# Kernel tuning notes

Hardware: AMD Instinct MI355X
Metric: run time of the kernel (lower is better)

Reference implementation:

```python
import jax, jax.numpy as jnp
import numpy as np

B, CIN, D, H, W = 2, 64, 64, 64, 64
NUM_CLASSES = 5
STRIDE = 2
NMAX = 32
TOPK = 13
TAL_ALPHA, TAL_BETA = 1.0, 6.0
EPS = 1e-9


def setup_inputs() -> dict:
    key = jax.random.key(0)
    ks = jax.random.split(key, 6)
    features = jax.random.normal(ks[0], (B, CIN, D, H, W), jnp.float32)
    cls_w = jax.random.normal(ks[1], (NUM_CLASSES, CIN, 3, 3, 3), jnp.float32) * 0.02
    cls_b = jnp.zeros((NUM_CLASSES,), jnp.float32)
    off_w = jax.random.normal(ks[2], (3, CIN, 3, 3, 3), jnp.float32) * 0.01
    off_b = jnp.zeros((3,), jnp.float32)
    coords = jax.random.uniform(ks[3], (B, NMAX, 3), jnp.float32, 4.0, float(D * STRIDE) - 4.0)
    cls = jax.random.randint(ks[4], (B, NMAX, 1), 0, NUM_CLASSES).astype(jnp.float32)
    sigma = jax.random.uniform(ks[5], (B, NMAX, 1), jnp.float32, 2.0, 8.0)
    pad = (jnp.arange(NMAX) >= 24)[None, :, None]  # last 8 GT slots are padding
    cls = jnp.where(pad, -100.0, cls)
    labels = jnp.concatenate([coords, cls, sigma], axis=-1)  # B N 5 : x,y,z,class,sigma
    return {"features": features, "cls_w": cls_w, "cls_b": cls_b,
            "off_w": off_w, "off_b": off_b, "labels": labels}


def conv3d(x, w, b):
    y = jax.lax.conv_general_dilated(x, w, (1, 1, 1), 'SAME',
                                     dimension_numbers=('NCDHW', 'OIDHW', 'NCDHW'))
    return y + b[None, :, None, None, None]


def make_anchors():
    g = jnp.stack(jnp.meshgrid(jnp.arange(D), jnp.arange(H), jnp.arange(W), indexing='ij'))
    return (g.astype(jnp.float32) + 0.5) * STRIDE  # (3, D, H, W)


def flatten_bchw(x):
    # B C D H W -> B (D H W) C
    Bsz, C = x.shape[0], x.shape[1]
    return x.transpose(0, 2, 3, 4, 1).reshape(Bsz, -1, C)


def tal_assign(pred_logits, pred_centers, true_labels, true_centers, true_sigmas, valid):
    # pred_logits (B,L,C); pred_centers (B,L,3); true_* (B,N,...); valid (B,N) bool
    Bsz, L, C = pred_logits.shape
    N = true_labels.shape[1]
    d2 = jnp.sum((true_centers[:, :, None, :] - pred_centers[:, None, :, :]) ** 2, -1)  # B N L
    ious = jnp.exp(-d2 / (2.0 * true_sigmas[:, :, None] ** 2))  # keypoint IoU, B N L
    probs = jax.nn.sigmoid(pred_logits).transpose(0, 2, 1)  # B C L
    cls_scores = jnp.take_along_axis(probs, true_labels[:, :, None], axis=1)  # B N L
    align = (cls_scores ** TAL_ALPHA) * (ious ** TAL_BETA)  # alignment metric
    topv, topi = jax.lax.top_k(align, TOPK)
    is_topk = jnp.zeros_like(align).at[
        jnp.arange(Bsz)[:, None, None], jnp.arange(N)[None, :, None], topi
    ].set(jnp.where(topv > EPS, 1.0, 0.0))
    mask_pos = is_topk * valid[:, :, None].astype(align.dtype)  # B N L
    pos_sum = mask_pos.sum(axis=1)  # B L
    # resolve anchors matched to multiple GTs: keep GT with max IoU
    is_max_iou = jax.nn.one_hot(jnp.argmax(ious, axis=1), N, axis=1, dtype=align.dtype)
    mask_pos = jnp.where(pos_sum[:, None, :] > 1, is_max_iou, mask_pos)
    pos_sum = mask_pos.sum(axis=1)
    fg = pos_sum > 0  # B L
    assigned_gt = jnp.argmax(mask_pos, axis=1)  # B L
    assigned_labels = jnp.take_along_axis(true_labels, assigned_gt, axis=1)
    assigned_labels = jnp.where(fg, assigned_labels, C)  # bg_index = C
    assigned_centers = jnp.take_along_axis(true_centers, assigned_gt[:, :, None], axis=1)  # B L 3
    assigned_sigmas = jnp.take_along_axis(true_sigmas, assigned_gt, axis=1)  # B L
    align = align * mask_pos
    max_align = align.max(axis=2, keepdims=True)  # B N 1
    max_iou = (ious * mask_pos).max(axis=2, keepdims=True)
    score = (align * max_iou / (max_align + EPS)).max(axis=1)  # B L
    assigned_scores = jax.nn.one_hot(assigned_labels, C + 1)[..., :C] * score[..., None]  # B L C
    return assigned_labels, assigned_centers, assigned_scores, assigned_sigmas


def detection_loss(logits, offsets, anchors, labels):
    pred_logits = flatten_bchw(logits)               # B L C
    pred_centers = flatten_bchw(anchors + offsets)   # B L 3
    anchor_pts = flatten_bchw(anchors)
    C = pred_logits.shape[-1]
    true_centers = labels[..., :3]
    true_labels_f = labels[..., 3]
    true_sigmas = labels[..., 4]
    valid = true_labels_f != -100.0
    true_labels = jnp.where(valid, true_labels_f, 0.0).astype(jnp.int32)
    assigned = tal_assign(jax.lax.stop_gradient(pred_logits),
                          jax.lax.stop_gradient(pred_centers),
                          true_labels, true_centers, true_sigmas, valid)
    assigned_labels, assigned_centers, assigned_scores, assigned_sigmas = jax.lax.stop_gradient(assigned)
    one_hot_label = jax.nn.one_hot(assigned_labels, C + 1)[..., :C]
    # varifocal loss (alpha=0.75, gamma=2)
    p = jax.nn.sigmoid(pred_logits)
    weight = 0.75 * (p ** 2.0) * (1.0 - one_hot_label) + assigned_scores * one_hot_label
    bce = assigned_scores * jax.nn.softplus(-pred_logits) + (1.0 - assigned_scores) * jax.nn.softplus(pred_logits)
    cls_loss = jnp.sum(weight * bce)
    d = jnp.sum((pred_centers - assigned_centers) ** 2, -1)  # B L
    w = assigned_scores.sum(-1)
    iou = jnp.exp(-d / (2.0 * assigned_sigmas ** 2))
    mask_positive = assigned_labels != C
    reg_loss = jnp.sum(jnp.where(mask_positive, (1.0 - iou) * w, 0.0))
    return (cls_loss + reg_loss) / assigned_scores.sum()


def reference(features, cls_w, cls_b, off_w, off_b, labels):
    logits = conv3d(features, cls_w, cls_b)    # B C D H W
    offsets = conv3d(features, off_w, off_b)   # B 3 D H W
    anchors = jnp.broadcast_to(make_anchors()[None], (features.shape[0], 3, D, H, W))
    loss = detection_loss(logits, offsets, anchors, labels)
    return loss
```

## Files before the change

kernel.cpp:

```cpp
#include <hip/hip_runtime.h>
#include <math.h>

#define NB 2
#define CIN 64
#define DD_ 64
#define HH_ 64
#define WW_ 64
#define NCLS 5
#define LL (DD_*HH_*WW_)
#define NMAXG 32
#define TOPKK 13
#define NSLAB 4

typedef __attribute__((ext_vector_type(8)))  short short8b;
typedef __attribute__((ext_vector_type(16))) float floatx16;

__device__ __forceinline__ float softplusf_(float z){
  return fmaxf(z, 0.f) + log1pf(expf(-fabsf(z)));
}
__device__ __forceinline__ float sigmoidf_(float z){
  return 1.f/(1.f + expf(-z));
}
__device__ __forceinline__ unsigned tobf_u_(float f){
  unsigned u = __float_as_uint(f);
  return (u + 0x7fffu + ((u>>16)&1u)) >> 16;
}
__device__ __forceinline__ short tobf_(float f){
  return (short)tobf_u_(f);
}

__global__ __launch_bounds__(256) void wtrans_kernel(
    const float* __restrict__ cls_w, const float* __restrict__ off_w,
    short* __restrict__ wA, float* __restrict__ bgz)
{
  if (blockIdx.x == 0 && threadIdx.x < 2) bgz[threadIdx.x] = 0.f;
  int idx = blockIdx.x*256 + threadIdx.x;
  if (idx >= 216*64) return;
  int slice = idx >> 6; int lane = idx & 63;
  int cc = slice & 3; int r = slice >> 2;
  int kw = r % 3; int r2 = r / 3;
  int kh = r2 % 3; int rr = r2 / 3;
  int m = lane & 31, khalf = lane >> 5;
  int outch = m & 7;
  int kd = rr - (m >> 3);
  short8b out;
  #pragma unroll
  for (int i=0;i<8;++i){
    int c = cc*16 + khalf*8 + i;
    float wv = 0.f;
    if (kd >= 0 && kd <= 2){
      if (outch < NCLS) wv = cls_w[(outch*CIN + c)*27 + kd*9 + kh*3 + kw];
      else              wv = off_w[((outch-NCLS)*CIN + c)*27 + kd*9 + kh*3 + kw];
    }
    out[i] = tobf_(wv);
  }
  *(short8b*)(wA + (size_t)idx*8) = out;
}

__global__ __launch_bounds__(256) void transpose_kernel(
    const float* __restrict__ feat, short* __restrict__ featT)
{
  const int t = threadIdx.x;
  const int w = t & 63;
  const int hh = t >> 6;
  const int d = blockIdx.x;
  const int h = blockIdx.y*4 + hh;
  const int b = blockIdx.z;
  const float* src = feat + (size_t)b*CIN*LL + (size_t)d*4096 + (size_t)h*64 + w;
  const size_t sp = (size_t)d*4096 + (size_t)h*64 + w;
  #pragma unroll
  for (int cc=0; cc<4; ++cc){
    float f[16];
    #pragma unroll
    for (int j=0;j<16;++j) f[j] = src[(size_t)(cc*16+j)*LL];
    uint4 p0, p1;
    p0.x = (tobf_u_(f[1])<<16)|tobf_u_(f[0]);  p0.y = (tobf_u_(f[3])<<16)|tobf_u_(f[2]);
    p0.z = (tobf_u_(f[5])<<16)|tobf_u_(f[4]);  p0.w = (tobf_u_(f[7])<<16)|tobf_u_(f[6]);
    p1.x = (tobf_u_(f[9])<<16)|tobf_u_(f[8]);  p1.y = (tobf_u_(f[11])<<16)|tobf_u_(f[10]);
    p1.z = (tobf_u_(f[13])<<16)|tobf_u_(f[12]);p1.w = (tobf_u_(f[15])<<16)|tobf_u_(f[14]);
    short* dst = featT + ((size_t)(b*4+cc)*LL + sp)*16;
    *(uint4*)(dst)     = p0;
    *(uint4*)(dst + 8) = p1;
  }
}

__global__ __launch_bounds__(256, 2) void conv_mfma_kernel(
    const short* __restrict__ featT,
    const short* __restrict__ wA,
    const float* __restrict__ cls_b, const float* __restrict__ off_b,
    float* __restrict__ logits_ws,
    float* __restrict__ centers_ws,
    float* __restrict__ bg_sum,
    unsigned* __restrict__ moff_u)
{
  __shared__ short xs[36*68*16];
  __shared__ float bsum[4];

  const int tid = threadIdx.x;
  const int lane = tid & 63, hl = tid >> 6;
  const int col = lane & 31, khalf = lane >> 5;
  const int h0 = blockIdx.x*4, d0 = blockIdx.y*4, b = blockIdx.z;

  for (int idx = tid; idx < 36*32; idx += 256){
    int row = idx >> 5; int rr2 = idx & 31;
    int wp = (rr2 < 16) ? 0 : 65;
    xs[(row*68 + wp)*16 + (rr2 & 15)] = 0;
  }

  floatx16 accA = (floatx16)(0.f);
  floatx16 accB = (floatx16)(0.f);

  const short8b* wAv = (const short8b*)wA;
  const bool edge = (d0==0) || (d0==DD_-4) || (h0==0) || (h0==HH_-4);

  #pragma unroll 1
  for (int cc=0; cc<4; ++cc){
    if (cc) __syncthreads();
    const short* plane = featT + (size_t)(b*4+cc)*LL*16;
    if (!edge){
      #pragma unroll 3
      for (int it=0; it<18; ++it){
        int idx = it*256 + tid;
        int half = idx & 1;
        int wp1  = ((idx>>1) & 63) + 1;
        int row  = idx >> 7;
        int row_d = row/6, row_h = row - row_d*6;
        const short* sp = plane + ((size_t)(d0-1+row_d)*4096 + (size_t)(h0-1+row_h)*64 + (wp1-1))*16 + half*8;
        uint4 pk = *(const uint4*)sp;
        *(uint4*)(xs + (row*68 + wp1)*16 + ((half ^ ((wp1>>2)&1))<<3)) = pk;
      }
    } else {
      #pragma unroll 3
      for (int it=0; it<18; ++it){
        int idx = it*256 + tid;
        int half = idx & 1;
        int wp1  = ((idx>>1) & 63) + 1;
        int row  = idx >> 7;
        int row_d = row/6, row_h = row - row_d*6;
        int d_ = d0 - 1 + row_d;
        int h_ = h0 - 1 + row_h;
        bool inb = ((unsigned)d_ < 64u) && ((unsigned)h_ < 64u);
        const short* sp = plane + ((size_t)(inb?d_:0)*4096 + (size_t)(inb?h_:0)*64 + (wp1-1))*16 + half*8;
        uint4 pk = make_uint4(0,0,0,0);
        if (inb) pk = *(const uint4*)sp;
        *(uint4*)(xs + (row*68 + wp1)*16 + ((half ^ ((wp1>>2)&1))<<3)) = pk;
      }
    }
    __syncthreads();
    #pragma unroll 1
    for (int rr=0; rr<6; ++rr){
      if ((unsigned)(d0 - 1 + rr) >= 64u) continue;
      short8b areg[9];
      #pragma unroll
      for (int q=0;q<9;++q)
        areg[q] = wAv[(size_t)((rr*9 + q)*4 + cc)*64 + lane];
      #pragma unroll
      for (int kh=0;kh<3;++kh){
        if ((unsigned)(h0 + hl - 1 + kh) >= 64u) continue;
        int row = rr*6 + hl + kh;
        #pragma unroll
        for (int kw=0;kw<3;++kw){
          short8b a = areg[kh*3+kw];
          {
            int wp = col + kw;
            int sidx = (row*68 + wp)*16 + ((khalf ^ ((wp>>2)&1))<<3);
            short8b bfr = *(const short8b*)(xs + sidx);
            accA = __builtin_amdgcn_mfma_f32_32x32x16_bf16(a, bfr, accA, 0,0,0);
          }
          {
            int wp = 32 + col + kw;
            int sidx = (row*68 + wp)*16 + ((khalf ^ ((wp>>2)&1))<<3);
            short8b bfr = *(const short8b*)(xs + sidx);
            accB = __builtin_amdgcn_mfma_f32_32x32x16_bf16(a, bfr, accB, 0,0,0);
          }
        }
      }
    }
  }

  float bg = 0.f, om = 0.f;
  const int h = h0 + hl;
  #pragma unroll
  for (int wh=0; wh<2; ++wh){
    const int w = wh*32 + col;
    #pragma unroll
    for (int dq=0; dq<4; ++dq){
      int d = d0 + dq;
      size_t l = (size_t)d*4096 + (size_t)h*64 + w;
      float v0 = wh ? accB[dq*4+0] : accA[dq*4+0];
      float v1 = wh ? accB[dq*4+1] : accA[dq*4+1];
      float v2 = wh ? accB[dq*4+2] : accA[dq*4+2];
      float v3 = wh ? accB[dq*4+3] : accA[dq*4+3];
      if (khalf == 0){
        float z0 = v0 + cls_b[0]; logits_ws[(size_t)(b*NCLS+0)*LL + l] = z0;
        float z1 = v1 + cls_b[1]; logits_ws[(size_t)(b*NCLS+1)*LL + l] = z1;
        float z2 = v2 + cls_b[2]; logits_ws[(size_t)(b*NCLS+2)*LL + l] = z2;
        float z3 = v3 + cls_b[3]; logits_ws[(size_t)(b*NCLS+3)*LL + l] = z3;
        float p;
        p = sigmoidf_(z0); bg += 0.75f*p*p*softplusf_(z0);
        p = sigmoidf_(z1); bg += 0.75f*p*p*softplusf_(z1);
        p = sigmoidf_(z2); bg += 0.75f*p*p*softplusf_(z2);
        p = sigmoidf_(z3); bg += 0.75f*p*p*softplusf_(z3);
      } else {
        float z4 = v0 + cls_b[4]; logits_ws[(size_t)(b*NCLS+4)*LL + l] = z4;
        float p = sigmoidf_(z4); bg += 0.75f*p*p*softplusf_(z4);
        float o0 = v1 + off_b[0];
        float o1 = v2 + off_b[1];
        float o2 = v3 + off_b[2];
        om = fmaxf(om, fmaxf(fabsf(o0), fmaxf(fabsf(o1), fabsf(o2))));
        float4 ctr;
        ctr.x = ((float)d+0.5f)*2.f + o0;
        ctr.y = ((float)h+0.5f)*2.f + o1;
        ctr.z = ((float)w+0.5f)*2.f + o2;
        ctr.w = 0.f;
        *(float4*)(centers_ws + ((size_t)b*LL + l)*4) = ctr;
      }
    }
  }
  #pragma unroll
  for (int off=32;off;off>>=1){
    bg += __shfl_down(bg, off);
    om = fmaxf(om, __shfl_xor(om, off));
  }
  if (lane == 0){
    bsum[hl] = bg;
    atomicMax(moff_u, __float_as_uint(om));
  }
  __syncthreads();
  if (tid == 0)
    atomicAdd(bg_sum, bsum[0]+bsum[1]+bsum[2]+bsum[3]);
}

__global__ __launch_bounds__(256) void topk_box_kernel(
    const float* __restrict__ logits_ws, const float* __restrict__ centers_ws,
    const float* __restrict__ labels,
    const unsigned* __restrict__ moff_u,
    float* __restrict__ pv, int* __restrict__ pi)
{
  const int bn = blockIdx.x;
  const int slab = blockIdx.y;
  const int b = bn >> 5, n = bn & 31;
  const int tid = threadIdx.x;

  const float* lb = labels + (b*NMAXG + n)*5;
  const float tx = lb[0], ty = lb[1], tz = lb[2];
  const float cf = lb[3];
  const float sg = lb[4];
  const int lab = (cf == -100.f) ? 0 : (int)cf;
  const float m6 = -3.f/(sg*sg);
  const float moff = __uint_as_float(*moff_u);
  const float R = 2.6336f*sg + moff + 0.05f;

  int i0d = (int)ceilf((tx - R - 1.f)*0.5f); if (i0d < 0) i0d = 0;
  int i1d = (int)floorf((tx + R - 1.f)*0.5f); if (i1d > 63) i1d = 63;
  int i0h = (int)ceilf((ty - R - 1.f)*0.5f); if (i0h < 0) i0h = 0;
  int i1h = (int)floorf((ty + R - 1.f)*0.5f); if (i1h > 63) i1h = 63;
  int i0w = (int)ceilf((tz - R - 1.f)*0.5f); if (i0w < 0) i0w = 0;
  int i1w = (int)floorf((tz + R - 1.f)*0.5f); if (i1w > 63) i1w = 63;
  int nd = i1d-i0d+1, nh = i1h-i0h+1, nw = i1w-i0w+1;
  int total = (nd>0 && nh>0 && nw>0) ? nd*nh*nw : 0;
  int lo = (total*slab)/NSLAB, hi = (total*(slab+1))/NSLAB;

  const float* lg = logits_ws + (size_t)(b*NCLS + lab)*LL;
  const float* cb = centers_ws + (size_t)b*LL*4;

  float v[13]; int ix[13];
  #pragma unroll
  for (int j=0;j<13;++j){ v[j]=-1.f; ix[j]=0x7fffffff; }

  for (int idx = lo + tid; idx < hi; idx += 256){
    int r = idx;
    int wi = r % nw; r /= nw;
    int hi2 = r % nh; int di = r / nh;
    int l = (i0d+di)*4096 + (i0h+hi2)*64 + (i0w+wi);
    float4 c4 = *(const float4*)(cb + (size_t)l*4);
    float dx = c4.x-tx, dy = c4.y-ty, dz = c4.z-tz;
    float e = m6*(dx*dx + dy*dy + dz*dz);
    if (e < -20.8f) continue;
    float a = sigmoidf_(lg[l]) * expf(e);
    if (a > v[12]){
      float cv = a; int ci = l;
      #pragma unroll
      for (int j=0;j<13;++j){
        bool take = (cv > v[j]) || (cv == v[j] && ci < ix[j]);
        float nv = take ? cv : v[j];  float ov = take ? v[j] : cv;
        int   ni = take ? ci : ix[j]; int   oi = take ? ix[j] : ci;
        v[j]=nv; ix[j]=ni; cv=ov; ci=oi;
      }
    }
  }

  const int lane = tid & 63, wvi = tid >> 6;
  float mv = -2.f; int mi = 0x7fffffff;
  #pragma unroll 1
  for (int k=0;k<13;++k){
    float bv = v[0]; int bi = ix[0]; int bl = lane;
    #pragma unroll
    for (int off=32; off; off>>=1){
      float ov2 = __shfl_xor(bv, off);
      int oi = __shfl_xor(bi, off);
      int ol = __shfl_xor(bl, off);
      if (ov2 > bv || (ov2 == bv && oi < bi)){ bv=ov2; bi=oi; bl=ol; }
    }
    if (lane == k){ mv = bv; mi = bi; }
    if (lane == bl){
      #pragma unroll
      for (int j=0;j<12;++j){ v[j]=v[j+1]; ix[j]=ix[j+1]; }
      v[12] = -2.f; ix[12] = 0x7fffffff;
    }
  }
  __shared__ float sv2[4*13]; __shared__ int si2[4*13];
  if (lane < 13){ sv2[wvi*13+lane] = mv; si2[wvi*13+lane] = mi; }
  __syncthreads();
  if (wvi == 0){
    float v2 = -2.f; int i2 = 0x7fffffff;
    if (lane < 52){ v2 = sv2[lane]; i2 = si2[lane]; }
    #pragma unroll 1
    for (int k=0;k<13;++k){
      float bv = v2; int bi = i2; int bl = lane;
      #pragma unroll
      for (int off=32; off; off>>=1){
        float ov2 = __shfl_xor(bv, off);
        int oi = __shfl_xor(bi, off);
        int ol = __shfl_xor(bl, off);
        if (ov2 > bv || (ov2 == bv && oi < bi)){ bv=ov2; bi=oi; bl=ol; }
      }
      if (lane == 0){
        pv[(bn*NSLAB+slab)*TOPKK + k] = bv;
        pi[(bn*NSLAB+slab)*TOPKK + k] = bi;
      }
      if (lane == bl) v2 = -2.f;
    }
  }
}

__global__ __launch_bounds__(64) void topk_merge_kernel(
    const float* __restrict__ pv, const int* __restrict__ pi,
    float* __restrict__ tv, int* __restrict__ ti)
{
  const int bn = blockIdx.x;
  const int t = threadIdx.x;
  const int NC = NSLAB*TOPKK;
  float v = -2.f; int ix = 0x7fffffff;
  if (t < NC){ v = pv[bn*NC + t]; ix = pi[bn*NC + t]; }
  #pragma unroll 1
  for (int k=0;k<13;++k){
    float bv = v; int bi = ix; int bl = t;
    #pragma unroll
    for (int off=32; off; off>>=1){
      float ov = __shfl_xor(bv, off);
      int oi = __shfl_xor(bi, off);
      int ol = __shfl_xor(bl, off);
      if (ov > bv || (ov == bv && oi < bi)){ bv=ov; bi=oi; bl=ol; }
    }
    if (t==0){ tv[bn*TOPKK+k]=bv; ti[bn*TOPKK+k]=bi; }
    if (t==bl) v = -2.f;
  }
}

__global__ __launch_bounds__(1024) void finalize_kernel(
    const float* __restrict__ logits_ws, const float* __restrict__ centers_ws,
    const float* __restrict__ labels,
    const float* __restrict__ tv, const int* __restrict__ ti,
    const float* __restrict__ bg_sum, float* __restrict__ out)
{
  const int tid = threadIdx.x;
  __shared__ float gx[64], gy[64], gz[64], gs[64];
  __shared__ int glab[64], gvalid[64];
  __shared__ int hkey[2048], hcnt[2048], hmin[2048];
  __shared__ unsigned maxA[64], maxI[64];
  __shared__ float accD, accC;
  if (tid==0){ accD=0.f; accC=0.f; }
  for (int i=tid;i<2048;i+=1024){ hkey[i]=-1; hcnt[i]=0; hmin[i]=0x7fffffff; }
  if (tid<64){
    const float* lb = labels + tid*5;
    gx[tid]=lb[0]; gy[tid]=lb[1]; gz[tid]=lb[2];
    float cf = lb[3]; gs[tid]=lb[4];
    int val = (cf != -100.f);
    gvalid[tid]=val; glab[tid]= val ? (int)cf : 0;
    maxA[tid]=0u; maxI[tid]=0u;
  }
  __syncthreads();

  const int e = tid;
  bool ok = false; int l = -1; int n = 0; int b = 0;
  if (e < 2*416){
    b = (e >= 416) ? 1 : 0;
    int eb = e - 416*b;
    n = eb/13; int k = eb - 13*n;
    float v = tv[(b*NMAXG+n)*TOPKK + k];
    l = ti[(b*NMAXG+n)*TOPKK + k];
    ok = gvalid[b*32+n] && (v > 1e-9f);
  }
  int slot = -1;
  if (ok){
    unsigned h = (((unsigned)l * 2654435761u) >> 20) & 1023u;
    for (;;){
      int prev = atomicCAS(&hkey[b*1024 + h], -1, l);
      if (prev == -1 || prev == l){ slot = b*1024 + (int)h; break; }
      h = (h+1) & 1023u;
    }
    atomicAdd(&hcnt[slot], 1);
    atomicMin(&hmin[slot], e);
  }
  __syncthreads();

  bool first = ok && (hmin[slot] == e);
  float a=0.f, iou=0.f; int nstar=0;
  if (first){
    float px = centers_ws[((size_t)b*LL + l)*4 + 0];
    float py = centers_ws[((size_t)b*LL + l)*4 + 1];
    float pz = centers_ws[((size_t)b*LL + l)*4 + 2];
    if (hcnt[slot] == 1){
      nstar = n;
    } else {
      float best = -1.f; int bidx = 0;
      #pragma unroll 1
      for (int nn=0;nn<32;++nn){
        float dx=gx[b*32+nn]-px, dy=gy[b*32+nn]-py, dz=gz[b*32+nn]-pz;
        float d2 = dx*dx+dy*dy+dz*dz;
        float io = expf(-d2/(2.f*gs[b*32+nn]*gs[b*32+nn]));
        if (io > best){ best=io; bidx=nn; }
      }
      nstar = bidx;
    }
    int gi = b*32 + nstar;
    float dx=gx[gi]-px, dy=gy[gi]-py, dz=gz[gi]-pz;
    float d2 = dx*dx+dy*dy+dz*dz;
    float sgv = gs[gi];
    iou = expf(-d2/(2.f*sgv*sgv));
    float z = logits_ws[(size_t)(b*NCLS + glab[gi])*LL + l];
    a = sigmoidf_(z) * expf(-3.f*d2/(sgv*sgv));
    atomicMax(&maxA[gi], __float_as_uint(a));
    atomicMax(&maxI[gi], __float_as_uint(iou));
  }
  __syncthreads();

  if (first){
    int gi = b*32 + nstar;
    float mA = __uint_as_float(maxA[gi]);
    float mI = __uint_as_float(maxI[gi]);
    float score = a*mI/(mA + 1e-9f);
    float z = logits_ws[(size_t)(b*NCLS + glab[gi])*LL + l];
    float p = sigmoidf_(z);
    float t2 = log1pf(expf(-fabsf(z)));
    float spz = fmaxf(z,0.f) + t2;
    float spm = fmaxf(-z,0.f) + t2;
    float corr = score*(score*spm + (1.f-score)*spz) - 0.75f*p*p*spz;
    float reg  = (1.f - iou)*score;
    atomicAdd(&accD, score);
    atomicAdd(&accC, corr + reg);
  }
  __syncthreads();
  if (tid==0) out[0] = (bg_sum[0] + accC) / accD;
}

extern "C" void kernel_launch(void* const* d_in, const int* in_sizes, int n_in,
                              void* d_out, int out_size, void* d_ws, size_t ws_size,
                              hipStream_t stream) {
  const float* feat  = (const float*)d_in[0];
  const float* cls_w = (const float*)d_in[1];
  const float* cls_b = (const float*)d_in[2];
  const float* off_w = (const float*)d_in[3];
  const float* off_b = (const float*)d_in[4];
  const float* labels= (const float*)d_in[5];
  float* out = (float*)d_out;

  float* logits_ws  = (float*)d_ws;
  float* centers_ws = logits_ws + (size_t)NB*NCLS*LL;
  float* tv = centers_ws + (size_t)NB*LL*4;
  int*   ti = (int*)(tv + 64*TOPKK);
  float* pv = (float*)(ti + 64*TOPKK);
  int*   pi = (int*)(pv + 64*NSLAB*TOPKK);
  float* bg = (float*)(pi + 64*NSLAB*TOPKK);
  short* wA = (short*)(bg + 16);
  short* featT = wA + 216*64*8;

  wtrans_kernel<<<54, 256, 0, stream>>>(cls_w, off_w, wA, bg);
  transpose_kernel<<<dim3(64,16,2), 256, 0, stream>>>(feat, featT);
  conv_mfma_kernel<<<dim3(16,16,2), 256, 0, stream>>>(
      featT, wA, cls_b, off_b, logits_ws, centers_ws, bg, (unsigned*)(bg+1));
  topk_box_kernel<<<dim3(64,NSLAB), 256, 0, stream>>>(
      logits_ws, centers_ws, labels, (const unsigned*)(bg+1), pv, pi);
  topk_merge_kernel<<<64, 64, 0, stream>>>(pv, pi, tv, ti);
  finalize_kernel<<<1, 1024, 0, stream>>>(
      logits_ws, centers_ws, labels, tv, ti, bg, out);
}
```

Baseline: 180.1 us.

## Split conv W-halves across 8 waves and drop top-k slab merge kernel

The conv kernel now runs 512 threads per block, so each wave computes one 32-wide W half with a single accumulator instead of two. This doubles the waves available to hide LDS and MFMA latency and halves accumulator register pressure, at the cost of each wave reloading the weight registers separately. The top-k stage drops the 4-slab split and its merge kernel: one block per GT object now scans the whole box. That removes a launch and the partial buffers, but gives the top-k stage a quarter as many blocks.

Result: slower. 225.4 us (+25.1%).

```diff
diff --git a/kernel.cpp b/kernel.cpp
--- a/kernel.cpp
+++ b/kernel.cpp
@@ -10,7 +10,6 @@
 #define LL (DD_*HH_*WW_)
 #define NMAXG 32
 #define TOPKK 13
-#define NSLAB 4
 
 typedef __attribute__((ext_vector_type(8)))  short short8b;
 typedef __attribute__((ext_vector_type(16))) float floatx16;
@@ -84,7 +83,7 @@
   }
 }
 
-__global__ __launch_bounds__(256, 2) void conv_mfma_kernel(
+__global__ __launch_bounds__(512, 2) void conv_mfma_kernel(
     const short* __restrict__ featT,
     const short* __restrict__ wA,
     const float* __restrict__ cls_b, const float* __restrict__ off_b,
@@ -94,21 +93,21 @@
     unsigned* __restrict__ moff_u)
 {
   __shared__ short xs[36*68*16];
-  __shared__ float bsum[4];
+  __shared__ float bsum[8];
 
   const int tid = threadIdx.x;
-  const int lane = tid & 63, hl = tid >> 6;
+  const int lane = tid & 63, wv = tid >> 6;
+  const int hl = wv >> 1, whalf = wv & 1;
   const int col = lane & 31, khalf = lane >> 5;
   const int h0 = blockIdx.x*4, d0 = blockIdx.y*4, b = blockIdx.z;
 
-  for (int idx = tid; idx < 36*32; idx += 256){
+  for (int idx = tid; idx < 36*32; idx += 512){
     int row = idx >> 5; int rr2 = idx & 31;
     int wp = (rr2 < 16) ? 0 : 65;
     xs[(row*68 + wp)*16 + (rr2 & 15)] = 0;
   }
 
-  floatx16 accA = (floatx16)(0.f);
-  floatx16 accB = (floatx16)(0.f);
+  floatx16 acc = (floatx16)(0.f);
 
   const short8b* wAv = (const short8b*)wA;
   const bool edge = (d0==0) || (d0==DD_-4) || (h0==0) || (h0==HH_-4);
@@ -118,9 +117,9 @@
     if (cc) __syncthreads();
     const short* plane = featT + (size_t)(b*4+cc)*LL*16;
     if (!edge){
-      #pragma unroll 3
-      for (int it=0; it<18; ++it){
-        int idx = it*256 + tid;
+      #pragma unroll
+      for (int it=0; it<9; ++it){
+        int idx = it*512 + tid;
         int half = idx & 1;
         int wp1  = ((idx>>1) & 63) + 1;
         int row  = idx >> 7;
@@ -130,9 +129,9 @@
         *(uint4*)(xs + (row*68 + wp1)*16 + ((half ^ ((wp1>>2)&1))<<3)) = pk;
       }
     } else {
-      #pragma unroll 3
-      for (int it=0; it<18; ++it){
-        int idx = it*256 + tid;
+      #pragma unroll
+      for (int it=0; it<9; ++it){
+        int idx = it*512 + tid;
         int half = idx & 1;
         int wp1  = ((idx>>1) & 63) + 1;
         int row  = idx >> 7;
@@ -161,18 +160,10 @@
         #pragma unroll
         for (int kw=0;kw<3;++kw){
           short8b a = areg[kh*3+kw];
-          {
-            int wp = col + kw;
-            int sidx = (row*68 + wp)*16 + ((khalf ^ ((wp>>2)&1))<<3);
-            short8b bfr = *(const short8b*)(xs + sidx);
-            accA = __builtin_amdgcn_mfma_f32_32x32x16_bf16(a, bfr, accA, 0,0,0);
-          }
-          {
-            int wp = 32 + col + kw;
-            int sidx = (row*68 + wp)*16 + ((khalf ^ ((wp>>2)&1))<<3);
-            short8b bfr = *(const short8b*)(xs + sidx);
-            accB = __builtin_amdgcn_mfma_f32_32x32x16_bf16(a, bfr, accB, 0,0,0);
-          }
+          int wp = whalf*32 + col + kw;
+          int sidx = (row*68 + wp)*16 + ((khalf ^ ((wp>>2)&1))<<3);
+          short8b bfr = *(const short8b*)(xs + sidx);
+          acc = __builtin_amdgcn_mfma_f32_32x32x16_bf16(a, bfr, acc, 0,0,0);
         }
       }
     }
@@ -180,41 +171,38 @@
 
   float bg = 0.f, om = 0.f;
   const int h = h0 + hl;
+  const int w = whalf*32 + col;
   #pragma unroll
-  for (int wh=0; wh<2; ++wh){
-    const int w = wh*32 + col;
-    #pragma unroll
-    for (int dq=0; dq<4; ++dq){
-      int d = d0 + dq;
-      size_t l = (size_t)d*4096 + (size_t)h*64 + w;
-      float v0 = wh ? accB[dq*4+0] : accA[dq*4+0];
-      float v1 = wh ? accB[dq*4+1] : accA[dq*4+1];
-      float v2 = wh ? accB[dq*4+2] : accA[dq*4+2];
-      float v3 = wh ? accB[dq*4+3] : accA[dq*4+3];
-      if (khalf == 0){
-        float z0 = v0 + cls_b[0]; logits_ws[(size_t)(b*NCLS+0)*LL + l] = z0;
-        float z1 = v1 + cls_b[1]; logits_ws[(size_t)(b*NCLS+1)*LL + l] = z1;
-        float z2 = v2 + cls_b[2]; logits_ws[(size_t)(b*NCLS+2)*LL + l] = z2;
-        float z3 = v3 + cls_b[3]; logits_ws[(size_t)(b*NCLS+3)*LL + l] = z3;
-        float p;
-        p = sigmoidf_(z0); bg += 0.75f*p*p*softplusf_(z0);
-        p = sigmoidf_(z1); bg += 0.75f*p*p*softplusf_(z1);
-        p = sigmoidf_(z2); bg += 0.75f*p*p*softplusf_(z2);
-        p = sigmoidf_(z3); bg += 0.75f*p*p*softplusf_(z3);
-      } else {
-        float z4 = v0 + cls_b[4]; logits_ws[(size_t)(b*NCLS+4)*LL + l] = z4;
-        float p = sigmoidf_(z4); bg += 0.75f*p*p*softplusf_(z4);
-        float o0 = v1 + off_b[0];
-        float o1 = v2 + off_b[1];
-        float o2 = v3 + off_b[2];
-        om = fmaxf(om, fmaxf(fabsf(o0), fmaxf(fabsf(o1), fabsf(o2))));
-        float4 ctr;
-        ctr.x = ((float)d+0.5f)*2.f + o0;
-        ctr.y = ((float)h+0.5f)*2.f + o1;
-        ctr.z = ((float)w+0.5f)*2.f + o2;
-        ctr.w = 0.f;
-        *(float4*)(centers_ws + ((size_t)b*LL + l)*4) = ctr;
-      }
+  for (int dq=0; dq<4; ++dq){
+    int d = d0 + dq;
+    size_t l = (size_t)d*4096 + (size_t)h*64 + w;
+    float v0 = acc[dq*4+0];
+    float v1 = acc[dq*4+1];
+    float v2 = acc[dq*4+2];
+    float v3 = acc[dq*4+3];
+    if (khalf == 0){
+      float z0 = v0 + cls_b[0]; logits_ws[(size_t)(b*NCLS+0)*LL + l] = z0;
+      float z1 = v1 + cls_b[1]; logits_ws[(size_t)(b*NCLS+1)*LL + l] = z1;
+      float z2 = v2 + cls_b[2]; logits_ws[(size_t)(b*NCLS+2)*LL + l] = z2;
+      float z3 = v3 + cls_b[3]; logits_ws[(size_t)(b*NCLS+3)*LL + l] = z3;
+      float p;
+      p = sigmoidf_(z0); bg += 0.75f*p*p*softplusf_(z0);
+      p = sigmoidf_(z1); bg += 0.75f*p*p*softplusf_(z1);
+      p = sigmoidf_(z2); bg += 0.75f*p*p*softplusf_(z2);
+      p = sigmoidf_(z3); bg += 0.75f*p*p*softplusf_(z3);
+    } else {
+      float z4 = v0 + cls_b[4]; logits_ws[(size_t)(b*NCLS+4)*LL + l] = z4;
+      float p = sigmoidf_(z4); bg += 0.75f*p*p*softplusf_(z4);
+      float o0 = v1 + off_b[0];
+      float o1 = v2 + off_b[1];
+      float o2 = v3 + off_b[2];
+      om = fmaxf(om, fmaxf(fabsf(o0), fmaxf(fabsf(o1), fabsf(o2))));
+      float4 ctr;
+      ctr.x = ((float)d+0.5f)*2.f + o0;
+      ctr.y = ((float)h+0.5f)*2.f + o1;
+      ctr.z = ((float)w+0.5f)*2.f + o2;
+      ctr.w = 0.f;
+      *(float4*)(centers_ws + ((size_t)b*LL + l)*4) = ctr;
     }
   }
   #pragma unroll
@@ -223,22 +211,25 @@
     om = fmaxf(om, __shfl_xor(om, off));
   }
   if (lane == 0){
-    bsum[hl] = bg;
+    bsum[wv] = bg;
     atomicMax(moff_u, __float_as_uint(om));
   }
   __syncthreads();
-  if (tid == 0)
-    atomicAdd(bg_sum, bsum[0]+bsum[1]+bsum[2]+bsum[3]);
+  if (tid == 0){
+    float s = 0.f;
+    #pragma unroll
+    for (int i=0;i<8;++i) s += bsum[i];
+    atomicAdd(bg_sum, s);
+  }
 }
 
 __global__ __launch_bounds__(256) void topk_box_kernel(
     const float* __restrict__ logits_ws, const float* __restrict__ centers_ws,
     const float* __restrict__ labels,
     const unsigned* __restrict__ moff_u,
-    float* __restrict__ pv, int* __restrict__ pi)
+    float* __restrict__ tv, int* __restrict__ ti)
 {
   const int bn = blockIdx.x;
-  const int slab = blockIdx.y;
   const int b = bn >> 5, n = bn & 31;
   const int tid = threadIdx.x;
 
@@ -259,7 +250,6 @@
   int i1w = (int)floorf((tz + R - 1.f)*0.5f); if (i1w > 63) i1w = 63;
   int nd = i1d-i0d+1, nh = i1h-i0h+1, nw = i1w-i0w+1;
   int total = (nd>0 && nh>0 && nw>0) ? nd*nh*nw : 0;
-  int lo = (total*slab)/NSLAB, hi = (total*(slab+1))/NSLAB;
 
   const float* lg = logits_ws + (size_t)(b*NCLS + lab)*LL;
   const float* cb = centers_ws + (size_t)b*LL*4;
@@ -268,7 +258,7 @@
   #pragma unroll
   for (int j=0;j<13;++j){ v[j]=-1.f; ix[j]=0x7fffffff; }
 
-  for (int idx = lo + tid; idx < hi; idx += 256){
+  for (int idx = tid; idx < total; idx += 256){
     int r = idx;
     int wi = r % nw; r /= nw;
     int hi2 = r % nh; int di = r / nh;
@@ -326,35 +316,11 @@
         if (ov2 > bv || (ov2 == bv && oi < bi)){ bv=ov2; bi=oi; bl=ol; }
       }
       if (lane == 0){
-        pv[(bn*NSLAB+slab)*TOPKK + k] = bv;
-        pi[(bn*NSLAB+slab)*TOPKK + k] = bi;
+        tv[bn*TOPKK + k] = bv;
+        ti[bn*TOPKK + k] = bi;
       }
       if (lane == bl) v2 = -2.f;
     }
-  }
-}
-
-__global__ __launch_bounds__(64) void topk_merge_kernel(
-    const float* __restrict__ pv, const int* __restrict__ pi,
-    float* __restrict__ tv, int* __restrict__ ti)
-{
-  const int bn = blockIdx.x;
-  const int t = threadIdx.x;
-  const int NC = NSLAB*TOPKK;
-  float v = -2.f; int ix = 0x7fffffff;
-  if (t < NC){ v = pv[bn*NC + t]; ix = pi[bn*NC + t]; }
-  #pragma unroll 1
-  for (int k=0;k<13;++k){
-    float bv = v; int bi = ix; int bl = t;
-    #pragma unroll
-    for (int off=32; off; off>>=1){
-      float ov = __shfl_xor(bv, off);
-      int oi = __shfl_xor(bi, off);
-      int ol = __shfl_xor(bl, off);
-      if (ov > bv || (ov == bv && oi < bi)){ bv=ov; bi=oi; bl=ol; }
-    }
-    if (t==0){ tv[bn*TOPKK+k]=bv; ti[bn*TOPKK+k]=bi; }
-    if (t==bl) v = -2.f;
   }
 }
 
@@ -470,19 +436,16 @@
   float* centers_ws = logits_ws + (size_t)NB*NCLS*LL;
   float* tv = centers_ws + (size_t)NB*LL*4;
   int*   ti = (int*)(tv + 64*TOPKK);
-  float* pv = (float*)(ti + 64*TOPKK);
-  int*   pi = (int*)(pv + 64*NSLAB*TOPKK);
-  float* bg = (float*)(pi + 64*NSLAB*TOPKK);
+  float* bg = (float*)(ti + 64*TOPKK);
   short* wA = (short*)(bg + 16);
   short* featT = wA + 216*64*8;
 
   wtrans_kernel<<<54, 256, 0, stream>>>(cls_w, off_w, wA, bg);
   transpose_kernel<<<dim3(64,16,2), 256, 0, stream>>>(feat, featT);
-  conv_mfma_kernel<<<dim3(16,16,2), 256, 0, stream>>>(
+  conv_mfma_kernel<<<dim3(16,16,2), 512, 0, stream>>>(
       featT, wA, cls_b, off_b, logits_ws, centers_ws, bg, (unsigned*)(bg+1));
-  topk_box_kernel<<<dim3(64,NSLAB), 256, 0, stream>>>(
-      logits_ws, centers_ws, labels, (const unsigned*)(bg+1), pv, pi);
-  topk_merge_kernel<<<64, 64, 0, stream>>>(pv, pi, tv, ti);
+  topk_box_kernel<<<64, 256, 0, stream>>>(
+      logits_ws, centers_ws, labels, (const unsigned*)(bg+1), tv, ti);
   finalize_kernel<<<1, 1024, 0, stream>>>(
       logits_ws, centers_ws, labels, tv, ti, bg, out);
 }
```

## Split channel halves into planes, use global_load_lds, double-buffer weight fragments

Applied to the files above, without the earlier changes.

The transposed feature layout now stores each 16-channel group as two separate 8-channel planes. The conv kernel can then stage tiles into LDS with direct global_load_lds DMA instead of going through registers. The LDS tile uses a split-half layout with padded rows in place of the XOR swizzle, and halo rows at the edges are zeroed once up front. Weight fragments are software-pipelined with two register sets so the next rr's loads overlap the current MFMAs, at the cost of higher register pressure and possible LDS bank conflicts from the new layout.

Result: faster. 170.5 us (-5.3%).

```diff
diff --git a/kernel.cpp b/kernel.cpp
--- a/kernel.cpp
+++ b/kernel.cpp
@@ -78,9 +78,8 @@
     p0.z = (tobf_u_(f[5])<<16)|tobf_u_(f[4]);  p0.w = (tobf_u_(f[7])<<16)|tobf_u_(f[6]);
     p1.x = (tobf_u_(f[9])<<16)|tobf_u_(f[8]);  p1.y = (tobf_u_(f[11])<<16)|tobf_u_(f[10]);
     p1.z = (tobf_u_(f[13])<<16)|tobf_u_(f[12]);p1.w = (tobf_u_(f[15])<<16)|tobf_u_(f[14]);
-    short* dst = featT + ((size_t)(b*4+cc)*LL + sp)*16;
-    *(uint4*)(dst)     = p0;
-    *(uint4*)(dst + 8) = p1;
+    *(uint4*)(featT + (((size_t)(b*4+cc)*2 + 0)*LL + sp)*8) = p0;
+    *(uint4*)(featT + (((size_t)(b*4+cc)*2 + 1)*LL + sp)*8) = p1;
   }
 }
 
@@ -93,89 +92,90 @@
     float* __restrict__ bg_sum,
     unsigned* __restrict__ moff_u)
 {
-  __shared__ short xs[36*68*16];
+  __shared__ short xs[36*132*8];
   __shared__ float bsum[4];
 
   const int tid = threadIdx.x;
   const int lane = tid & 63, hl = tid >> 6;
   const int col = lane & 31, khalf = lane >> 5;
   const int h0 = blockIdx.x*4, d0 = blockIdx.y*4, b = blockIdx.z;
-
-  for (int idx = tid; idx < 36*32; idx += 256){
-    int row = idx >> 5; int rr2 = idx & 31;
-    int wp = (rr2 < 16) ? 0 : 65;
-    xs[(row*68 + wp)*16 + (rr2 & 15)] = 0;
+  const bool edge = (d0==0) || (d0==DD_-4) || (h0==0) || (h0==HH_-4);
+
+  for (int idx = tid; idx < 144; idx += 256){
+    int row = idx >> 2, q = idx & 3;
+    *(uint4*)(xs + (row*132 + (q>>1)*66 + (q&1)*65)*8) = make_uint4(0,0,0,0);
+  }
+  if (edge){
+    #pragma unroll 1
+    for (int row=0; row<36; ++row){
+      int d_ = d0-1+row/6, h_ = h0-1+row-6*(row/6);
+      if ((unsigned)d_ < 64u && (unsigned)h_ < 64u) continue;
+      for (int idx = tid; idx < 128; idx += 256){
+        *(uint4*)(xs + (row*132 + (idx>>6)*66 + (idx&63) + 1)*8) = make_uint4(0,0,0,0);
+      }
+    }
   }
 
   floatx16 accA = (floatx16)(0.f);
   floatx16 accB = (floatx16)(0.f);
 
   const short8b* wAv = (const short8b*)wA;
-  const bool edge = (d0==0) || (d0==DD_-4) || (h0==0) || (h0==HH_-4);
+
+  int vA[3], vB[3];
+  #pragma unroll
+  for (int kw=0;kw<3;++kw){
+    vA[kw] = hl*0 + khalf*528 + (col+kw)*8;
+    vB[kw] = vA[kw] + 256;
+  }
+
+#define LOADA(dst, ccv, rrv) { \
+  _Pragma("unroll") \
+  for (int q=0;q<9;++q) dst[q] = wAv[(size_t)((((rrv)*9+q)*4+(ccv)))*64 + lane]; }
+
+#define COMPR(areg, rrv) \
+  if ((unsigned)(d0-1+(rrv)) < 64u){ \
+    _Pragma("unroll") \
+    for (int kh=0;kh<3;++kh){ \
+      if ((unsigned)(h0+hl-1+kh) < 64u){ \
+        const int rowb = ((rrv)*6 + hl + kh)*1056; \
+        _Pragma("unroll") \
+        for (int kw=0;kw<3;++kw){ \
+          short8b a = areg[kh*3+kw]; \
+          short8b b0 = *(const short8b*)(xs + rowb + vA[kw]); \
+          accA = __builtin_amdgcn_mfma_f32_32x32x16_bf16(a, b0, accA, 0,0,0); \
+          short8b b1 = *(const short8b*)(xs + rowb + vB[kw]); \
+          accB = __builtin_amdgcn_mfma_f32_32x32x16_bf16(a, b1, accB, 0,0,0); \
+        } } } }
+
+  short8b aP[9], aQ[9];
+  LOADA(aP, 0, 0);
 
   #pragma unroll 1
   for (int cc=0; cc<4; ++cc){
     if (cc) __syncthreads();
-    const short* plane = featT + (size_t)(b*4+cc)*LL*16;
-    if (!edge){
-      #pragma unroll 3
+    {
+      const short* plane = featT + (size_t)(b*4+cc)*2*(size_t)LL*8;
+      #pragma unroll
       for (int it=0; it<18; ++it){
-        int idx = it*256 + tid;
-        int half = idx & 1;
-        int wp1  = ((idx>>1) & 63) + 1;
-        int row  = idx >> 7;
-        int row_d = row/6, row_h = row - row_d*6;
-        const short* sp = plane + ((size_t)(d0-1+row_d)*4096 + (size_t)(h0-1+row_h)*64 + (wp1-1))*16 + half*8;
-        uint4 pk = *(const uint4*)sp;
-        *(uint4*)(xs + (row*68 + wp1)*16 + ((half ^ ((wp1>>2)&1))<<3)) = pk;
-      }
-    } else {
-      #pragma unroll 3
-      for (int it=0; it<18; ++it){
-        int idx = it*256 + tid;
-        int half = idx & 1;
-        int wp1  = ((idx>>1) & 63) + 1;
-        int row  = idx >> 7;
-        int row_d = row/6, row_h = row - row_d*6;
-        int d_ = d0 - 1 + row_d;
-        int h_ = h0 - 1 + row_h;
-        bool inb = ((unsigned)d_ < 64u) && ((unsigned)h_ < 64u);
-        const short* sp = plane + ((size_t)(inb?d_:0)*4096 + (size_t)(inb?h_:0)*64 + (wp1-1))*16 + half*8;
-        uint4 pk = make_uint4(0,0,0,0);
-        if (inb) pk = *(const uint4*)sp;
-        *(uint4*)(xs + (row*68 + wp1)*16 + ((half ^ ((wp1>>2)&1))<<3)) = pk;
+        int strip = it*4 + hl;
+        int row = strip >> 1, kh2 = strip & 1;
+        int d_ = d0 - 1 + row/6, h_ = h0 - 1 + row - 6*(row/6);
+        if (!edge || ((unsigned)d_ < 64u && (unsigned)h_ < 64u)){
+          const short* src = plane + ((size_t)kh2*LL + (size_t)d_*4096 + (size_t)h_*64 + lane)*8;
+          short* dst = xs + (row*132 + kh2*66 + 1)*8;
+          __builtin_amdgcn_global_load_lds(
+            (const __attribute__((address_space(1))) void*)src,
+            (__attribute__((address_space(3))) void*)dst, 16, 0, 0);
+        }
       }
     }
     __syncthreads();
-    #pragma unroll 1
-    for (int rr=0; rr<6; ++rr){
-      if ((unsigned)(d0 - 1 + rr) >= 64u) continue;
-      short8b areg[9];
-      #pragma unroll
-      for (int q=0;q<9;++q)
-        areg[q] = wAv[(size_t)((rr*9 + q)*4 + cc)*64 + lane];
-      #pragma unroll
-      for (int kh=0;kh<3;++kh){
-        if ((unsigned)(h0 + hl - 1 + kh) >= 64u) continue;
-        int row = rr*6 + hl + kh;
-        #pragma unroll
-        for (int kw=0;kw<3;++kw){
-          short8b a = areg[kh*3+kw];
-          {
-            int wp = col + kw;
-            int sidx = (row*68 + wp)*16 + ((khalf ^ ((wp>>2)&1))<<3);
-            short8b bfr = *(const short8b*)(xs + sidx);
-            accA = __builtin_amdgcn_mfma_f32_32x32x16_bf16(a, bfr, accA, 0,0,0);
-          }
-          {
-            int wp = 32 + col + kw;
-            int sidx = (row*68 + wp)*16 + ((khalf ^ ((wp>>2)&1))<<3);
-            short8b bfr = *(const short8b*)(xs + sidx);
-            accB = __builtin_amdgcn_mfma_f32_32x32x16_bf16(a, bfr, accB, 0,0,0);
-          }
-        }
-      }
-    }
+    LOADA(aQ, cc, 1);             COMPR(aP, 0);
+    LOADA(aP, cc, 2);             COMPR(aQ, 1);
+    LOADA(aQ, cc, 3);             COMPR(aP, 2);
+    LOADA(aP, cc, 4);             COMPR(aQ, 3);
+    LOADA(aQ, cc, 5);             COMPR(aP, 4);
+    { int nc = (cc+1)&3; LOADA(aP, nc, 0); }  COMPR(aQ, 5);
   }
 
   float bg = 0.f, om = 0.f;
```
